# Optimization experiments

Hardware: AMD Instinct MI355X
Metric: run time of the kernel (lower is better)

Reference implementation:

```python
import jax, jax.numpy as jnp
import numpy as np
from jax import lax

DN = ('NCHW', 'OIHW', 'NCHW')


def conv2d(x, w, b, stride, pad):
    y = lax.conv_general_dilated(x, w, (stride, stride), [(pad, pad), (pad, pad)],
                                 dimension_numbers=DN)
    return y + b[None, :, None, None]


def conv2d_transpose(x, w, b):
    # k=4, s=2, p=1 transposed conv: lhs_dilation=2, padding k-1-p=2.
    # w is stored directly as OIHW for this dilated conv (reference params).
    y = lax.conv_general_dilated(x, w, (1, 1), [(2, 2), (2, 2)],
                                 lhs_dilation=(2, 2), dimension_numbers=DN)
    return y + b[None, :, None, None]


def setup_inputs() -> dict:
    key = jax.random.key(0)
    ks = jax.random.split(key, 16)
    D, K = 64, 512  # embedding_dim, num_embeddings
    C1, C2 = 128, 256

    def w(k, shape, fan_in):
        return (jax.random.normal(k, shape, jnp.float32) / np.sqrt(fan_in)).astype(jnp.float32)

    inp = {
        'x':   jax.random.normal(ks[0], (8, 3, 256, 256), jnp.float32),
        # encoder: two stride-2 conv stages (k=4,s=2,p=1) + ReLU
        'ew1': w(ks[1], (C1, 3, 4, 4), 3 * 16),   'eb1': jnp.zeros((C1,), jnp.float32),
        'ew2': w(ks[2], (C2, C1, 4, 4), C1 * 16), 'eb2': jnp.zeros((C2,), jnp.float32),
        # pre_vq 1x1 conv: C2 -> D
        'pvw': w(ks[3], (D, C2, 1, 1), C2),       'pvb': jnp.zeros((D,), jnp.float32),
        # codebook, uniform(-1/K, 1/K) as in the torch init
        'emb': jax.random.uniform(ks[4], (K, D), jnp.float32, -1.0 / K, 1.0 / K),
        # post_vq 3x3 conv: D -> C2
        'qvw': w(ks[5], (C2, D, 3, 3), D * 9),    'qvb': jnp.zeros((C2,), jnp.float32),
        # decoder: two stride-2 transposed conv stages
        'dw1': w(ks[6], (C1, C2, 4, 4), C2 * 16), 'db1': jnp.zeros((C1,), jnp.float32),
        'dw2': w(ks[7], (3, C1, 4, 4), C1 * 16),  'db2': jnp.zeros((3,), jnp.float32),
    }
    return inp


def vector_quantize(z_e, emb, commitment_cost):
    # z_e: [B, D, H, W] -> [B, H, W, D]
    inputs = jnp.transpose(z_e, (0, 2, 3, 1))
    B, H, W, D = inputs.shape
    K = emb.shape[0]
    flat = inputs.reshape(-1, D)                                   # [N, D]
    dist = (jnp.sum(flat * flat, axis=1, keepdims=True)
            + jnp.sum(emb * emb, axis=1)
            - 2.0 * jnp.matmul(flat, emb.T))                        # [N, K]
    idx = jnp.argmin(dist, axis=1)                                  # [N]
    encodings = jax.nn.one_hot(idx, K, dtype=flat.dtype)            # [N, K]
    quantized = emb[idx].reshape(B, H, W, D)                        # gather == encodings @ emb

    e_latent_loss = jnp.mean((lax.stop_gradient(quantized) - inputs) ** 2)
    q_latent_loss = jnp.mean((quantized - lax.stop_gradient(inputs)) ** 2)
    loss = q_latent_loss + commitment_cost * e_latent_loss

    quantized_st = inputs + lax.stop_gradient(quantized - inputs)   # straight-through
    avg_probs = jnp.mean(encodings, axis=0)
    perplexity = jnp.exp(-jnp.sum(avg_probs * jnp.log(avg_probs + 1e-10)))
    return loss, jnp.transpose(quantized_st, (0, 3, 1, 2)), perplexity, encodings


def reference(x, ew1, eb1, ew2, eb2, pvw, pvb, emb, qvw, qvb, dw1, db1, dw2, db2):
    commitment_cost = 0.25
    # encode
    h = jax.nn.relu(conv2d(x, ew1, eb1, 2, 1))    # [8,128,128,128]
    h = jax.nn.relu(conv2d(h, ew2, eb2, 2, 1))    # [8,256,64,64]
    z_e = conv2d(h, pvw, pvb, 1, 0)               # [8,64,64,64]
    # vector quantize
    loss, quantized, perplexity, _ = vector_quantize(z_e, emb, commitment_cost)
    # decode
    g = conv2d(quantized, qvw, qvb, 1, 1)         # [8,256,64,64]
    g = jax.nn.relu(conv2d_transpose(g, dw1, db1))  # [8,128,128,128]
    x_recon = conv2d_transpose(g, dw2, db2)       # [8,3,256,256]
    return (loss, x_recon, perplexity)
```

## Files before the change

kernel.cpp:

```cpp
#include <hip/hip_runtime.h>
#include <math.h>

typedef unsigned short u16;
typedef unsigned int uint;
typedef __attribute__((ext_vector_type(8))) short bh8;
typedef __attribute__((ext_vector_type(4))) float f32x4;

#define DEV __device__ __forceinline__

DEV u16 f2bf(float x) {
  uint u = __builtin_bit_cast(uint, x);
  return (u16)((u + 0x7FFFu + ((u >> 16) & 1u)) >> 16);
}
DEV float bf2f(u16 h) { return __builtin_bit_cast(float, (uint)h << 16); }

DEV int xcd_swz(int bid, int nb) {
  int c = nb >> 3;
  return (bid & 7) * c + (bid >> 3);
}

__global__ __launch_bounds__(256, 2) void conv1_mfma3(const float* __restrict__ src,
                                                      const u16* __restrict__ B1h,
                                                      const u16* __restrict__ B1l,
                                                      const float* __restrict__ bias,
                                                      uint* __restrict__ outu) {
  __shared__ __align__(16) u16 Ah[128*72 + 32];
  __shared__ __align__(16) u16 Al[128*72 + 32];
  __shared__ __align__(16) u16 Bh[128*72 + 32];
  __shared__ __align__(16) u16 Bl[128*72 + 32];

  const int t = threadIdx.x;
  const int mt = xcd_swz((int)blockIdx.x, (int)gridDim.x);
  const int pl = t & 127, kb = t >> 7;
  const int p = mt*128 + pl;
  const int n = p >> 14, h = (p >> 7) & 127, w = p & 127;
  const int lane = t & 63, wv = t >> 6;
  const int lr = lane & 15, lg = lane >> 4;
  const int wm = wv & 1, wn = wv >> 1;

  uint hi16[16], lo16[16];
  #pragma unroll
  for (int q = 0; q < 16; ++q) {
    uint hh = 0, ll = 0;
    #pragma unroll
    for (int e = 0; e < 2; ++e) {
      const int k = kb*32 + q*2 + e;
      float val = 0.f;
      if (k < 48) {
        const int ic = k >> 4, r = k & 15;
        const int ih = 2*h - 1 + (r >> 2), iw = 2*w - 1 + (r & 3);
        if ((unsigned)ih < 256u && (unsigned)iw < 256u)
          val = src[((n*3 + ic) << 16) + (ih << 8) + iw];
      }
      u16 hi = f2bf(val);
      u16 lo = f2bf(val - bf2f(hi));
      hh |= (uint)hi << (16*e);
      ll |= (uint)lo << (16*e);
    }
    hi16[q] = hh; lo16[q] = ll;
  }
  const int aw = pl*72 + kb*32;
  #pragma unroll
  for (int i = 0; i < 4; ++i) {
    *(uint4*)&Ah[aw + i*8] = *(uint4*)&hi16[4*i];
    *(uint4*)&Al[aw + i*8] = *(uint4*)&lo16[4*i];
  }
  #pragma unroll
  for (int i = 0; i < 4; ++i) {
    int id = i*256 + t, oc = id >> 3, ch = id & 7;
    *(uint4*)&Bh[oc*72 + ch*8] = *(const uint4*)(B1h + (size_t)oc*64 + ch*8);
    *(uint4*)&Bl[oc*72 + ch*8] = *(const uint4*)(B1l + (size_t)oc*64 + ch*8);
  }
  __syncthreads();

  f32x4 acc[4][4];
  #pragma unroll
  for (int fm = 0; fm < 4; ++fm)
    #pragma unroll
    for (int fn = 0; fn < 4; ++fn)
      #pragma unroll
      for (int q = 0; q < 4; ++q) acc[fm][fn][q] = 0.f;

  #pragma unroll
  for (int ks = 0; ks < 2; ++ks) {
    bh8 afh[4], afl[4];
    #pragma unroll
    for (int fm = 0; fm < 4; ++fm) {
      const int r = (wm*64 + fm*16 + lr)*72 + ks*32 + lg*8;
      afh[fm] = *(const bh8*)&Ah[r];
      afl[fm] = *(const bh8*)&Al[r];
    }
    #pragma unroll
    for (int fn = 0; fn < 4; ++fn) {
      const int r = (wn*64 + fn*16 + lr)*72 + ks*32 + lg*8;
      bh8 bfh = *(const bh8*)&Bh[r];
      bh8 bfl = *(const bh8*)&Bl[r];
      #pragma unroll
      for (int fm = 0; fm < 4; ++fm) {
        acc[fm][fn] = __builtin_amdgcn_mfma_f32_16x16x32_bf16(afh[fm], bfh, acc[fm][fn], 0,0,0);
        acc[fm][fn] = __builtin_amdgcn_mfma_f32_16x16x32_bf16(afl[fm], bfh, acc[fm][fn], 0,0,0);
        acc[fm][fn] = __builtin_amdgcn_mfma_f32_16x16x32_bf16(afh[fm], bfl, acc[fm][fn], 0,0,0);
      }
    }
  }

  #pragma unroll
  for (int fm = 0; fm < 4; ++fm) {
    const int pq = mt*128 + wm*64 + fm*16 + lg*4;
    const int nn = pq >> 14, hh2 = (pq >> 7) & 127, ww = pq & 127;
    const int wh = ww >> 1;
    #pragma unroll
    for (int fn = 0; fn < 4; ++fn) {
      const int oc = wn*64 + fn*16 + lr;
      const float bv = bias[oc];
      uint pk[4];
      #pragma unroll
      for (int q = 0; q < 4; ++q) {
        float v = fmaxf(acc[fm][fn][q] + bv, 0.f);
        u16 hi = f2bf(v);
        u16 lo = f2bf(v - bf2f(hi));
        pk[q] = (uint)hi | ((uint)lo << 16);
      }
      uint* bp = outu + (size_t)(nn*128 + oc)*16384 + hh2*128;
      *(uint2*)(bp + wh)      = make_uint2(pk[0], pk[2]);
      *(uint2*)(bp + 64 + wh) = make_uint2(pk[1], pk[3]);
    }
  }
}

__global__ __launch_bounds__(256, 2) void conv2_mfma3(const uint* __restrict__ h1u,
                                                      const u16* __restrict__ Bh,
                                                      const u16* __restrict__ Bl,
                                                      const float* __restrict__ bias,
                                                      float* __restrict__ out) {
  __shared__ __align__(16) u16 Ah[128*72 + 32];
  __shared__ __align__(16) u16 Al[128*72 + 32];
  __shared__ __align__(16) u16 Bhs[128*72 + 32];
  __shared__ __align__(16) u16 Bls[128*72 + 32];

  const int t = threadIdx.x;
  const int bid = xcd_swz((int)blockIdx.x, (int)gridDim.x);
  const int nt = bid & 1, mt = bid >> 1;
  const int pl = t & 127, kb = t >> 7;
  const int p = mt*128 + pl;
  const int n = p >> 12, h = (p >> 6) & 63, w = p & 63;
  const int lane = t & 63, wv = t >> 6;
  const int lr = lane & 15, lg = lane >> 4;
  const int wm = wv & 1, wn = wv >> 1;

  int off[4]; uint mskd[4];
  off[0] = 64 + w - 1; mskd[0] = (w >= 1)  ? ~0u : 0u;
  off[1] = w;          mskd[1] = ~0u;
  off[2] = 64 + w;     mskd[2] = ~0u;
  off[3] = w + 1;      mskd[3] = (w <= 62) ? ~0u : 0u;

  f32x4 acc[4][4];
  #pragma unroll
  for (int fm = 0; fm < 4; ++fm)
    #pragma unroll
    for (int fn = 0; fn < 4; ++fn)
      #pragma unroll
      for (int q = 0; q < 4; ++q) acc[fm][fn][q] = 0.f;

  const int aw = pl*72 + kb*32;

  for (int k0 = 0; k0 < 2048; k0 += 64) {
    const int dy = k0 >> 9, icb = (k0 >> 2) & 127;
    const int ih = 2*h - 1 + dy;
    const uint mih = ((unsigned)ih < 128u) ? ~0u : 0u;
    const uint* pb = h1u + (size_t)(n*128 + icb + kb*8)*16384
                        + (((unsigned)ih < 128u) ? ih : 0)*128;
    uint m2[4];
    #pragma unroll
    for (int dx = 0; dx < 4; ++dx) m2[dx] = mskd[dx] & mih;

    uint raw[32];
    #pragma unroll
    for (int c = 0; c < 8; ++c)
      #pragma unroll
      for (int dx = 0; dx < 4; ++dx)
        raw[c*4 + dx] = pb[c*16384 + off[dx]] & m2[dx];

    uint hi16[16], lo16[16];
    #pragma unroll
    for (int q = 0; q < 16; ++q) {
      uint a = raw[2*q], b = raw[2*q+1];
      hi16[q] = (a & 0xffffu) | (b << 16);
      lo16[q] = (a >> 16) | (b & 0xffff0000u);
    }
    __syncthreads();
    #pragma unroll
    for (int i = 0; i < 4; ++i) {
      *(uint4*)&Ah[aw + i*8] = *(uint4*)&hi16[4*i];
      *(uint4*)&Al[aw + i*8] = *(uint4*)&lo16[4*i];
    }
    #pragma unroll
    for (int i = 0; i < 4; ++i) {
      int id = i*256 + t, oc = id >> 3, ch = id & 7;
      size_t bo = (size_t)(nt*128 + oc)*2048 + k0 + ch*8;
      *(uint4*)&Bhs[oc*72 + ch*8] = *(const uint4*)(Bh + bo);
      *(uint4*)&Bls[oc*72 + ch*8] = *(const uint4*)(Bl + bo);
    }
    __syncthreads();

    #pragma unroll
    for (int ks = 0; ks < 2; ++ks) {
      bh8 afh[4], afl[4];
      #pragma unroll
      for (int fm = 0; fm < 4; ++fm) {
        const int r = (wm*64 + fm*16 + lr)*72 + ks*32 + lg*8;
        afh[fm] = *(const bh8*)&Ah[r];
        afl[fm] = *(const bh8*)&Al[r];
      }
      #pragma unroll
      for (int fn = 0; fn < 4; ++fn) {
        const int r = (wn*64 + fn*16 + lr)*72 + ks*32 + lg*8;
        bh8 bfh = *(const bh8*)&Bhs[r];
        bh8 bfl = *(const bh8*)&Bls[r];
        #pragma unroll
        for (int fm = 0; fm < 4; ++fm) {
          acc[fm][fn] = __builtin_amdgcn_mfma_f32_16x16x32_bf16(afh[fm], bfh, acc[fm][fn], 0,0,0);
          acc[fm][fn] = __builtin_amdgcn_mfma_f32_16x16x32_bf16(afl[fm], bfh, acc[fm][fn], 0,0,0);
          acc[fm][fn] = __builtin_amdgcn_mfma_f32_16x16x32_bf16(afh[fm], bfl, acc[fm][fn], 0,0,0);
        }
      }
    }
  }

  #pragma unroll
  for (int fm = 0; fm < 4; ++fm) {
    const int pq = mt*128 + wm*64 + fm*16 + lg*4;
    const int nn = pq >> 12, hwq = pq & 4095;
    #pragma unroll
    for (int fn = 0; fn < 4; ++fn) {
      const int oc = nt*128 + wn*64 + fn*16 + lr;
      const float bv = bias[oc];
      float v0 = fmaxf(acc[fm][fn][0] + bv, 0.f);
      float v1 = fmaxf(acc[fm][fn][1] + bv, 0.f);
      float v2 = fmaxf(acc[fm][fn][2] + bv, 0.f);
      float v3 = fmaxf(acc[fm][fn][3] + bv, 0.f);
      *(float4*)(out + (((size_t)(nn*256 + oc)) << 12) + hwq) = make_float4(v0,v1,v2,v3);
    }
  }
}

__global__ __launch_bounds__(256, 2) void prevq_vq(const float* __restrict__ h2,
                                                   const float* __restrict__ btp,
                                                   const float* __restrict__ pvb,
                                                   const float* __restrict__ emb,
                                                   const u16* __restrict__ Ebh,
                                                   const u16* __restrict__ Ebl,
                                                   const float* __restrict__ enrm,
                                                   uint* __restrict__ qz32,
                                                   int* __restrict__ hist,
                                                   float* __restrict__ loss_sum) {
  __shared__ __align__(16) char SMEM[75776];
  float* Zs    = (float*)SMEM;
  u16*   Zh    = (u16*)(SMEM + 17408);
  u16*   Zl    = (u16*)(SMEM + 26624);
  u16*   Eh    = (u16*)(SMEM + 35840);
  u16*   El    = (u16*)(SMEM + 54272);
  float* nrmS  = (float*)(SMEM + 72704);
  float* wredv = (float*)(SMEM + 73216);
  int*   wredi = (int*)(SMEM + 74240);
  int*   sIdx  = (int*)(SMEM + 75264);
  float* As    = (float*)(SMEM + 35840);
  float* Bs    = (float*)(SMEM + 35840 + 4096);

  const int t = threadIdx.x;
  const int base = (int)blockIdx.x * 64;
  const int n = base >> 12, hwb = base & 4095;
  const int ti = t & 15, tj = t >> 4;

  {
    const int pl = t & 63, kb = t >> 6;
    const int hw = hwb + pl;
    float acc[4][4];
    #pragma unroll
    for (int i = 0; i < 4; ++i)
      #pragma unroll
      for (int j = 0; j < 4; ++j) acc[i][j] = 0.f;

    for (int k0 = 0; k0 < 256; k0 += 16) {
      #pragma unroll
      for (int jj = 0; jj < 4; ++jj) {
        int kr = jj*4 + kb;
        As[kr*64 + pl] = h2[((size_t)(n*256 + k0 + kr) << 12) + hw];
      }
      {
        int kr = t >> 4, c4 = t & 15;
        ((float4*)Bs)[kr*16 + c4] = *((const float4*)(btp + (size_t)(k0 + kr)*64) + c4);
      }
      __syncthreads();
      #pragma unroll
      for (int kk = 0; kk < 16; ++kk) {
        float a[4], b[4];
        *(float4*)&a[0] = *(const float4*)&As[kk*64 + ti*4];
        *(float4*)&b[0] = *(const float4*)&Bs[kk*64 + tj*4];
        #pragma unroll
        for (int i = 0; i < 4; ++i)
          #pragma unroll
          for (int j = 0; j < 4; ++j)
            acc[i][j] += a[i]*b[j];
      }
      __syncthreads();
    }
    #pragma unroll
    for (int j = 0; j < 4; ++j) {
      const int d = tj*4 + j;
      const float bvv = pvb[d];
      #pragma unroll
      for (int i = 0; i < 4; ++i) {
        const int px = ti*4 + i;
        float z = acc[i][j] + bvv;
        Zs[d*68 + px] = z;
        u16 h = f2bf(z);
        Zh[px*72 + d] = h;
        Zl[px*72 + d] = f2bf(z - bf2f(h));
      }
    }
  }

  const int lane = t & 63, wv = t >> 6;
  const int lr = lane & 15, lg = lane >> 4;

  float bv2[4][4]; int bi2[4][4];
  #pragma unroll
  for (int fm = 0; fm < 4; ++fm)
    #pragma unroll
    for (int q = 0; q < 4; ++q) { bv2[fm][q] = 3.402823466e38f; bi2[fm][q] = 0; }

  for (int c = 0; c < 4; ++c) {
    __syncthreads();
    #pragma unroll
    for (int i = 0; i < 4; ++i) {
      int id = i*256 + t, row = id >> 3, ch = id & 7;
      *(uint4*)&Eh[row*72 + ch*8] = *(const uint4*)(Ebh + (size_t)(c*128 + row)*64 + ch*8);
      *(uint4*)&El[row*72 + ch*8] = *(const uint4*)(Ebl + (size_t)(c*128 + row)*64 + ch*8);
    }
    if (t < 128) nrmS[t] = enrm[c*128 + t];
    __syncthreads();

    f32x4 acc2[4][2];
    #pragma unroll
    for (int fm = 0; fm < 4; ++fm)
      #pragma unroll
      for (int fn = 0; fn < 2; ++fn)
        #pragma unroll
        for (int q = 0; q < 4; ++q) acc2[fm][fn][q] = 0.f;

    #pragma unroll
    for (int ks = 0; ks < 2; ++ks) {
      bh8 ah[4], al[4];
      #pragma unroll
      for (int fm = 0; fm < 4; ++fm) {
        const int r = (fm*16 + lr)*72 + ks*32 + lg*8;
        ah[fm] = *(const bh8*)&Zh[r];
        al[fm] = *(const bh8*)&Zl[r];
      }
      #pragma unroll
      for (int fn = 0; fn < 2; ++fn) {
        const int r = (wv*32 + fn*16 + lr)*72 + ks*32 + lg*8;
        bh8 bh_ = *(const bh8*)&Eh[r];
        bh8 bl_ = *(const bh8*)&El[r];
        #pragma unroll
        for (int fm = 0; fm < 4; ++fm) {
          acc2[fm][fn] = __builtin_amdgcn_mfma_f32_16x16x32_bf16(ah[fm], bh_, acc2[fm][fn], 0,0,0);
          acc2[fm][fn] = __builtin_amdgcn_mfma_f32_16x16x32_bf16(al[fm], bh_, acc2[fm][fn], 0,0,0);
          acc2[fm][fn] = __builtin_amdgcn_mfma_f32_16x16x32_bf16(ah[fm], bl_, acc2[fm][fn], 0,0,0);
        }
      }
    }
    #pragma unroll
    for (int fn = 0; fn < 2; ++fn) {
      const int code = c*128 + wv*32 + fn*16 + lr;
      const float nv = nrmS[wv*32 + fn*16 + lr];
      #pragma unroll
      for (int fm = 0; fm < 4; ++fm)
        #pragma unroll
        for (int q = 0; q < 4; ++q) {
          float d = nv - 2.f*acc2[fm][fn][q];
          if (d < bv2[fm][q]) { bv2[fm][q] = d; bi2[fm][q] = code; }
        }
    }
  }

  #pragma unroll
  for (int fm = 0; fm < 4; ++fm)
    #pragma unroll
    for (int q = 0; q < 4; ++q) {
      float v = bv2[fm][q]; int ix = bi2[fm][q];
      #pragma unroll
      for (int m = 1; m < 16; m <<= 1) {
        float ov = __shfl_xor(v, m, 64);
        int   oi = __shfl_xor(ix, m, 64);
        if (ov < v || (ov == v && oi < ix)) { v = ov; ix = oi; }
      }
      if (lr == 0) {
        const int px = fm*16 + lg*4 + q;
        wredv[wv*64 + px] = v;
        wredi[wv*64 + px] = ix;
      }
    }
  __syncthreads();
  if (t < 64) {
    float best = 3.402823466e38f; int bid = 0x7fffffff;
    #pragma unroll
    for (int w2 = 0; w2 < 4; ++w2) {
      float v = wredv[w2*64 + t]; int ix = wredi[w2*64 + t];
      if (v < best || (v == best && ix < bid)) { best = v; bid = ix; }
    }
    sIdx[t] = bid;
  }
  __syncthreads();

  const int px = t & 63, grp = t >> 6;
  const int ix = sIdx[px];
  const float* er = emb + (size_t)ix * 64 + grp*16;
  uint* qb = qz32 + ((size_t)(n*32 + grp*8))*4096 + hwb + px;
  float ls = 0.f;
  #pragma unroll
  for (int dp = 0; dp < 8; ++dp) {
    float e0 = er[2*dp], e1 = er[2*dp + 1];
    float z0 = Zs[(grp*16 + 2*dp)*68 + px];
    float z1 = Zs[(grp*16 + 2*dp + 1)*68 + px];
    float d0 = e0 - z0, d1 = e1 - z1;
    ls += d0*d0 + d1*d1;
    qb[(size_t)dp * 4096] = (uint)f2bf(e0) | ((uint)f2bf(e1) << 16);
  }
  if (t < 64) atomicAdd(&hist[ix], 1);
  #pragma unroll
  for (int o = 32; o; o >>= 1) ls += __shfl_down(ls, o, 64);
  if ((t & 63) == 0) atomicAdd(loss_sum, ls);
}

__global__ void finalize_kernel(const int* __restrict__ hist,
                                const float* __restrict__ loss_sum,
                                float* __restrict__ out_loss,
                                float* __restrict__ out_perp) {
  __shared__ float red[512];
  int t = threadIdx.x;
  float pr = (float)hist[t] * (1.f/32768.f);
  red[t] = pr * logf(pr + 1e-10f);
  __syncthreads();
  for (int s = 256; s; s >>= 1) {
    if (t < s) red[t] += red[t + s];
    __syncthreads();
  }
  if (t == 0) {
    out_loss[0] = 1.25f * loss_sum[0] * (1.f/2097152.f);
    out_perp[0] = expf(-red[0]);
  }
}

enum { M_POSTVQ, M_DECONV1, M_DECONV2 };

template<int MODE>
__global__ __launch_bounds__(256, 4) void dec_mfma128(const uint* __restrict__ srcu,
                                                      const u16* __restrict__ Bt,
                                                      const float* __restrict__ bias,
                                                      uint* __restrict__ out32) {
  constexpr int K = (MODE == M_POSTVQ) ? 576 : 1024;
  __shared__ __align__(16) u16 As[128*72 + 32];
  __shared__ __align__(16) u16 Bs[128*72 + 32];

  const int t = threadIdx.x;
  int bid = xcd_swz((int)blockIdx.x, (int)gridDim.x);
  int par = 0, nt = 0, mt;
  if constexpr (MODE == M_DECONV1) { par = bid & 3; mt = bid >> 2; }
  else                             { nt = bid & 1;  mt = bid >> 1; }
  const u16* Brow = Bt + (size_t)((MODE == M_DECONV1) ? par*128 : nt*128) * K;

  const int pl = t & 127, kb = t >> 7;
  const int p = mt*128 + pl;
  const int n = p >> 12, h = (p >> 6) & 63, w = p & 63;
  const int lane = t & 63, wv = t >> 6;
  const int lr = lane & 15, lg = lane >> 4;
  const int wm = wv & 1, wn = wv >> 1;

  f32x4 acc[4][4];
  #pragma unroll
  for (int fm = 0; fm < 4; ++fm)
    #pragma unroll
    for (int fn = 0; fn < 4; ++fn)
      #pragma unroll
      for (int q = 0; q < 4; ++q) acc[fm][fn][q] = 0.f;

  const int aw = pl*72 + kb*32;

  for (int k0 = 0; k0 < K; k0 += 64) {
    const uint* up; bool ok;
    if constexpr (MODE == M_POSTVQ) {
      int r = k0 >> 6, kh = r / 3, kw = r - 3*kh;
      int ih = h - 1 + kh, iw = w - 1 + kw;
      ok = ((unsigned)ih < 64u) && ((unsigned)iw < 64u);
      up = srcu + ((size_t)(n*32 + kb*16)) * 4096
                + (ok ? ((ih << 6) + iw) : 0);
    } else {
      int j = k0 >> 8, icb = k0 & 255;
      int j1 = j >> 1, j0 = j & 1;
      int py = par >> 1, px = par & 1;
      int ih = h + py - 1 + j1, iw = w + px - 1 + j0;
      ok = ((unsigned)ih < 64u) && ((unsigned)iw < 64u);
      up = srcu + ((size_t)(n*128 + (icb >> 1) + kb*16)) * 4096
                + (ok ? ((ih << 6) + iw) : 0);
    }
    uint raw[16];
    #pragma unroll
    for (int i = 0; i < 16; ++i)
      raw[i] = ok ? up[(size_t)i * 4096] : 0u;

    __syncthreads();
    #pragma unroll
    for (int i = 0; i < 4; ++i)
      *(uint4*)&As[aw + i*8] =
          make_uint4(raw[4*i], raw[4*i+1], raw[4*i+2], raw[4*i+3]);

    #pragma unroll
    for (int i = 0; i < 4; ++i) {
      int id = i*256 + t, oc = id >> 3, ch = id & 7;
      *(uint4*)&Bs[oc*72 + ch*8] = *(const uint4*)(Brow + (size_t)oc*K + k0 + ch*8);
    }
    __syncthreads();

    #pragma unroll
    for (int ks = 0; ks < 2; ++ks) {
      bh8 af[4];
      #pragma unroll
      for (int fm = 0; fm < 4; ++fm)
        af[fm] = *(const bh8*)&As[(wm*64 + fm*16 + lr)*72 + ks*32 + lg*8];
      #pragma unroll
      for (int fn = 0; fn < 4; ++fn) {
        bh8 bf = *(const bh8*)&Bs[(wn*64 + fn*16 + lr)*72 + ks*32 + lg*8];
        #pragma unroll
        for (int fm = 0; fm < 4; ++fm)
          acc[fm][fn] = __builtin_amdgcn_mfma_f32_16x16x32_bf16(af[fm], bf, acc[fm][fn], 0, 0, 0);
      }
    }
  }

  const bool evn = !(lr & 1);
  #pragma unroll
  for (int fm = 0; fm < 4; ++fm) {
    const int pq = mt*128 + wm*64 + fm*16 + lg*4;
    const int nn = pq >> 12, hwq = pq & 4095;
    #pragma unroll
    for (int fn = 0; fn < 4; ++fn) {
      const int oc = nt*128 + wn*64 + fn*16 + lr;
      const float bvv = bias[oc];
      float v[4];
      #pragma unroll
      for (int q = 0; q < 4; ++q) {
        v[q] = acc[fm][fn][q] + bvv;
        if constexpr (MODE == M_DECONV1) v[q] = fmaxf(v[q], 0.f);
      }
      float pv[4];
      #pragma unroll
      for (int q = 0; q < 4; ++q) pv[q] = __shfl_xor(v[q], 1, 64);
      uint pk[4];
      #pragma unroll
      for (int q = 0; q < 4; ++q) {
        u16 a = f2bf(evn ? v[q] : pv[q]);
        u16 b = f2bf(evn ? pv[q] : v[q]);
        pk[q] = (uint)a | ((uint)b << 16);
      }
      size_t pbase;
      if constexpr (MODE == M_POSTVQ)
        pbase = ((size_t)(nn*128 + (oc >> 1))) * 4096 + hwq;
      else
        pbase = ((size_t)((nn*4 + par)*64 + (oc >> 1))) * 4096 + hwq;
      if (evn) *(uint2*)(out32 + pbase)     = make_uint2(pk[0], pk[1]);
      else     *(uint2*)(out32 + pbase + 2) = make_uint2(pk[2], pk[3]);
    }
  }
}

__global__ __launch_bounds__(256, 4) void deconv2_mfma(const uint* __restrict__ srcu,
                                                       const u16* __restrict__ Bt,
                                                       const float* __restrict__ bias,
                                                       float* __restrict__ outf) {
  constexpr int K = 512, BN = 16;
  __shared__ __align__(16) u16 As[128 * 72];
  __shared__ __align__(16) u16 Bs[BN * 72];

  const int t = threadIdx.x;
  int bid = xcd_swz((int)blockIdx.x, (int)gridDim.x);
  int par = bid & 3; bid >>= 2;
  const int mt = bid;
  const u16* Brow = Bt + (size_t)par * BN * K;

  const int pl = t & 127, kb = t >> 7;
  const int p = mt * 128 + pl;
  const int n = p >> 14, h = (p >> 7) & 127, w = p & 127;

  const int lane = t & 63, wv = t >> 6;
  const int lr = lane & 15, lg = lane >> 4;

  f32x4 acc[2];
  #pragma unroll
  for (int fm = 0; fm < 2; ++fm)
    #pragma unroll
    for (int q = 0; q < 4; ++q) acc[fm][q] = 0.f;

  for (int k0 = 0; k0 < K; k0 += 64) {
    int tap = k0 >> 7, icb = k0 & 127;
    int j1 = tap >> 1, j0 = tap & 1;
    int qy = par >> 1, qx = par & 1;
    int ih = h - 1 + qy + j1, iw = w - 1 + qx + j0;
    bool ok = ((unsigned)ih < 128u) && ((unsigned)iw < 128u);
    int ipar = ((ih & 1) << 1) | (iw & 1);
    const uint* up = srcu + ((size_t)((n*4 + ipar)*64 + (icb >> 1) + kb*16)) * 4096
                          + (ok ? (((ih >> 1) << 6) + (iw >> 1)) : 0);
    uint raw[16];
    #pragma unroll
    for (int i = 0; i < 16; ++i)
      raw[i] = ok ? up[(size_t)i * 4096] : 0u;

    __syncthreads();
    #pragma unroll
    for (int i = 0; i < 4; ++i)
      *(uint4*)&As[pl*72 + kb*32 + i*8] =
          make_uint4(raw[4*i], raw[4*i+1], raw[4*i+2], raw[4*i+3]);
    {
      int id = t;
      if (id < BN*8) {
        int oc = id >> 3, ch = id & 7;
        *(uint4*)&Bs[oc*72 + ch*8] = *(const uint4*)(Brow + (size_t)oc*K + k0 + ch*8);
      }
    }
    __syncthreads();

    #pragma unroll
    for (int ks = 0; ks < 2; ++ks) {
      bh8 af[2];
      #pragma unroll
      for (int fm = 0; fm < 2; ++fm)
        af[fm] = *(const bh8*)&As[(wv*32 + fm*16 + lr)*72 + ks*32 + lg*8];
      bh8 bf = *(const bh8*)&Bs[lr*72 + ks*32 + lg*8];
      #pragma unroll
      for (int fm = 0; fm < 2; ++fm)
        acc[fm] = __builtin_amdgcn_mfma_f32_16x16x32_bf16(af[fm], bf, acc[fm], 0, 0, 0);
    }
  }

  #pragma unroll
  for (int fm = 0; fm < 2; ++fm) {
    const int pq = mt*128 + wv*32 + fm*16 + lg*4;
    const int oc = lr;
    if (oc < 3) {
      const float bvv = bias[oc];
      const int nn = pq >> 14;
      const int hq = (pq >> 7) & 127, wq = pq & 127;
      const int qy = par >> 1, qx = par & 1;
      const int oh = 2*hq + qy;
      float* ob = outf + (((size_t)(nn*3 + oc)) << 16) + (oh << 8) + qx;
      ob[2*wq]     = acc[fm][0] + bvv;
      ob[2*wq + 2] = acc[fm][1] + bvv;
      ob[2*wq + 4] = acc[fm][2] + bvv;
      ob[2*wq + 6] = acc[fm][3] + bvv;
    }
  }
}

__global__ void prep_all(const float* __restrict__ ew1, const float* __restrict__ ew2,
                         const float* __restrict__ pvw, const float* __restrict__ emb,
                         const float* __restrict__ qvw, const float* __restrict__ dw1,
                         const float* __restrict__ dw2,
                         u16* bt1h, u16* bt1l, u16* bt2h, u16* bt2l, float* btp,
                         u16* Ebh, u16* Ebl, float* enrm,
                         u16* btq, u16* btd, u16* btd2,
                         int* hist, float* lsum) {
  int i = blockIdx.x * 256 + threadIdx.x;
  if (i < 8192) {
    int oc = i >> 6, k = i & 63;
    float v = (k < 48) ? ew1[oc*48 + k] : 0.f;
    u16 hi = f2bf(v);
    bt1h[i] = hi;
    bt1l[i] = f2bf(v - bf2f(hi));
  } else if ((i -= 8192) < 524288) {
    int oc = i >> 11, k = i & 2047;
    int dy = k >> 9, ic = (k >> 2) & 127, dx = k & 3;
    float v = ew2[oc*2048 + ic*16 + dy*4 + dx];
    u16 hi = f2bf(v);
    bt2h[i] = hi;
    bt2l[i] = f2bf(v - bf2f(hi));
  } else if ((i -= 524288) < 16384) {
    int k = i >> 6, oc = i & 63;
    btp[i] = pvw[oc*256 + k];
  } else if ((i -= 16384) < 32768) {
    float v = emb[i];
    u16 hi = f2bf(v);
    Ebh[i] = hi;
    Ebl[i] = f2bf(v - bf2f(hi));
  } else if ((i -= 32768) < 512) {
    float s = 0.f;
    const float* er = emb + (size_t)i * 64;
    #pragma unroll
    for (int d = 0; d < 64; ++d) s += er[d]*er[d];
    enrm[i] = s;
  } else if ((i -= 512) < 147456) {
    int oc = i / 576, rem = i - oc*576, r = rem >> 6, ic = rem & 63;
    btq[i] = f2bf(qvw[oc*576 + ic*9 + r]);
  } else if ((i -= 147456) < 524288) {
    int pr = i >> 17, oc = (i >> 10) & 127, j = (i >> 8) & 3, ic = i & 255;
    int py = pr >> 1, px = pr & 1, j1 = j >> 1, j0 = j & 1;
    btd[i] = f2bf(dw1[oc*4096 + ic*16 + (py + 2*j1)*4 + (px + 2*j0)]);
  } else if ((i -= 524288) < 32768) {
    int q = i >> 13, oc = (i >> 9) & 15, tap = (i >> 7) & 3, ic = i & 127;
    int qy = q >> 1, qx = q & 1, j1 = tap >> 1, j0 = tap & 1;
    btd2[i] = (oc < 3) ? f2bf(dw2[oc*2048 + ic*16 + (qy + 2*j1)*4 + (qx + 2*j0)]) : (u16)0;
  } else if ((i -= 32768) < 528) {
    if (i < 512) hist[i] = 0;
    else         lsum[i - 512] = 0.f;
  }
}

extern "C" void kernel_launch(void* const* d_in, const int* in_sizes, int n_in,
                              void* d_out, int out_size, void* d_ws, size_t ws_size,
                              hipStream_t stream) {
  (void)in_sizes; (void)n_in; (void)ws_size;
  const float* x   = (const float*)d_in[0];
  const float* ew1 = (const float*)d_in[1];
  const float* eb1 = (const float*)d_in[2];
  const float* ew2 = (const float*)d_in[3];
  const float* eb2 = (const float*)d_in[4];
  const float* pvw = (const float*)d_in[5];
  const float* pvb = (const float*)d_in[6];
  const float* emb = (const float*)d_in[7];
  const float* qvw = (const float*)d_in[8];
  const float* qvb = (const float*)d_in[9];
  const float* dw1 = (const float*)d_in[10];
  const float* db1 = (const float*)d_in[11];
  const float* dw2 = (const float*)d_in[12];
  const float* db2 = (const float*)d_in[13];
  float* out = (float*)d_out;

  char* ws = (char*)d_ws;
  uint*  h1u  = (uint*) (ws);
  float* h2   = (float*)(ws + 67108864);
  uint*  qz32 = (uint*) (ws + 109051904);
  int*   hist = (int*)  (ws + 113246208);
  float* lsum = (float*)(ws + 113248256);
  u16*   bt1h = (u16*)  (ws + 113248320);
  u16*   bt1l = (u16*)  (ws + 113264704);
  float* btp  = (float*)(ws + 113281088);
  u16*   bt2h = (u16*)  (ws + 113346624);
  u16*   bt2l = (u16*)  (ws + 114395200);
  u16*   btq  = (u16*)  (ws + 115443776);
  u16*   btd  = (u16*)  (ws + 115738688);
  u16*   btd2 = (u16*)  (ws + 116787264);
  u16*   Ebh  = (u16*)  (ws + 116852800);
  u16*   Ebl  = (u16*)  (ws + 116918336);
  float* enrm = (float*)(ws + 116983872);
  uint* g32  = (uint*)(ws + 67108864);
  uint* g232 = (uint*)ws;

  prep_all<<<5029, 256, 0, stream>>>(ew1, ew2, pvw, emb, qvw, dw1, dw2,
                                     bt1h, bt1l, bt2h, bt2l, btp,
                                     Ebh, Ebl, enrm, btq, btd, btd2, hist, lsum);

  conv1_mfma3<<<1024, 256, 0, stream>>>(x, bt1h, bt1l, eb1, h1u);
  conv2_mfma3<<<512, 256, 0, stream>>>(h1u, bt2h, bt2l, eb2, h2);

  prevq_vq<<<512, 256, 0, stream>>>(h2, btp, pvb, emb, Ebh, Ebl, enrm, qz32, hist, lsum);
  finalize_kernel<<<1, 512, 0, stream>>>(hist, lsum, out, out + (out_size - 1));

  dec_mfma128<M_POSTVQ> <<<512,  256, 0, stream>>>(qz32, btq, qvb, g32);
  dec_mfma128<M_DECONV1><<<1024, 256, 0, stream>>>(g32, btd, db1, g232);
  deconv2_mfma<<<4096, 256, 0, stream>>>(g232, btd2, db2, out + 1);
}
```

Measured before the change: 378.1 us.

## Run pre-VQ 1x1 conv on split-bf16 MFMA with packed hi/lo conv2 output

```diff
diff --git a/kernel.cpp b/kernel.cpp
--- a/kernel.cpp
+++ b/kernel.cpp
@@ -132,7 +132,7 @@
                                                       const u16* __restrict__ Bh,
                                                       const u16* __restrict__ Bl,
                                                       const float* __restrict__ bias,
-                                                      float* __restrict__ out) {
+                                                      uint* __restrict__ outh2) {
   __shared__ __align__(16) u16 Ah[128*72 + 32];
   __shared__ __align__(16) u16 Al[128*72 + 32];
   __shared__ __align__(16) u16 Bhs[128*72 + 32];
@@ -235,17 +235,23 @@
     for (int fn = 0; fn < 4; ++fn) {
       const int oc = nt*128 + wn*64 + fn*16 + lr;
       const float bv = bias[oc];
-      float v0 = fmaxf(acc[fm][fn][0] + bv, 0.f);
-      float v1 = fmaxf(acc[fm][fn][1] + bv, 0.f);
-      float v2 = fmaxf(acc[fm][fn][2] + bv, 0.f);
-      float v3 = fmaxf(acc[fm][fn][3] + bv, 0.f);
-      *(float4*)(out + (((size_t)(nn*256 + oc)) << 12) + hwq) = make_float4(v0,v1,v2,v3);
-    }
-  }
-}
-
-__global__ __launch_bounds__(256, 2) void prevq_vq(const float* __restrict__ h2,
-                                                   const float* __restrict__ btp,
+      uint pk[4];
+      #pragma unroll
+      for (int q = 0; q < 4; ++q) {
+        float v = fmaxf(acc[fm][fn][q] + bv, 0.f);
+        u16 hi = f2bf(v);
+        u16 lo = f2bf(v - bf2f(hi));
+        pk[q] = (uint)hi | ((uint)lo << 16);
+      }
+      *(uint4*)(outh2 + (((size_t)(nn*256 + oc)) << 12) + hwq) =
+          make_uint4(pk[0], pk[1], pk[2], pk[3]);
+    }
+  }
+}
+
+__global__ __launch_bounds__(256, 2) void prevq_vq(const uint* __restrict__ h2u,
+                                                   const u16* __restrict__ btph,
+                                                   const u16* __restrict__ btpl,
                                                    const float* __restrict__ pvb,
                                                    const float* __restrict__ emb,
                                                    const u16* __restrict__ Ebh,
@@ -258,71 +264,85 @@
   float* Zs    = (float*)SMEM;
   u16*   Zh    = (u16*)(SMEM + 17408);
   u16*   Zl    = (u16*)(SMEM + 26624);
+  u16*   A1h   = (u16*)(SMEM + 35840);
+  u16*   A1l   = (u16*)(SMEM + 45056);
+  u16*   B1h   = (u16*)(SMEM + 54272);
+  u16*   B1l   = (u16*)(SMEM + 63488);
   u16*   Eh    = (u16*)(SMEM + 35840);
   u16*   El    = (u16*)(SMEM + 54272);
   float* nrmS  = (float*)(SMEM + 72704);
   float* wredv = (float*)(SMEM + 73216);
   int*   wredi = (int*)(SMEM + 74240);
   int*   sIdx  = (int*)(SMEM + 75264);
-  float* As    = (float*)(SMEM + 35840);
-  float* Bs    = (float*)(SMEM + 35840 + 4096);
 
   const int t = threadIdx.x;
   const int base = (int)blockIdx.x * 64;
   const int n = base >> 12, hwb = base & 4095;
-  const int ti = t & 15, tj = t >> 4;
-
-  {
-    const int pl = t & 63, kb = t >> 6;
-    const int hw = hwb + pl;
-    float acc[4][4];
-    #pragma unroll
-    for (int i = 0; i < 4; ++i)
-      #pragma unroll
-      for (int j = 0; j < 4; ++j) acc[i][j] = 0.f;
-
-    for (int k0 = 0; k0 < 256; k0 += 16) {
-      #pragma unroll
-      for (int jj = 0; jj < 4; ++jj) {
-        int kr = jj*4 + kb;
-        As[kr*64 + pl] = h2[((size_t)(n*256 + k0 + kr) << 12) + hw];
-      }
-      {
-        int kr = t >> 4, c4 = t & 15;
-        ((float4*)Bs)[kr*16 + c4] = *((const float4*)(btp + (size_t)(k0 + kr)*64) + c4);
-      }
-      __syncthreads();
-      #pragma unroll
-      for (int kk = 0; kk < 16; ++kk) {
-        float a[4], b[4];
-        *(float4*)&a[0] = *(const float4*)&As[kk*64 + ti*4];
-        *(float4*)&b[0] = *(const float4*)&Bs[kk*64 + tj*4];
-        #pragma unroll
-        for (int i = 0; i < 4; ++i)
-          #pragma unroll
-          for (int j = 0; j < 4; ++j)
-            acc[i][j] += a[i]*b[j];
-      }
-      __syncthreads();
-    }
-    #pragma unroll
-    for (int j = 0; j < 4; ++j) {
-      const int d = tj*4 + j;
-      const float bvv = pvb[d];
-      #pragma unroll
-      for (int i = 0; i < 4; ++i) {
-        const int px = ti*4 + i;
-        float z = acc[i][j] + bvv;
-        Zs[d*68 + px] = z;
-        u16 h = f2bf(z);
-        Zh[px*72 + d] = h;
-        Zl[px*72 + d] = f2bf(z - bf2f(h));
-      }
-    }
-  }
-
   const int lane = t & 63, wv = t >> 6;
   const int lr = lane & 15, lg = lane >> 4;
+
+  {
+    const int px = t & 63, kb = t >> 6;
+    f32x4 acc1[4];
+    #pragma unroll
+    for (int fm = 0; fm < 4; ++fm)
+      #pragma unroll
+      for (int q = 0; q < 4; ++q) acc1[fm][q] = 0.f;
+
+    for (int k0 = 0; k0 < 256; k0 += 64) {
+      const uint* pb = h2u + ((size_t)(n*256 + k0 + kb*16)) * 4096 + hwb + px;
+      uint raw[16];
+      #pragma unroll
+      for (int c = 0; c < 16; ++c) raw[c] = pb[(size_t)c * 4096];
+      uint hi8[8], lo8[8];
+      #pragma unroll
+      for (int q = 0; q < 8; ++q) {
+        uint a = raw[2*q], b = raw[2*q+1];
+        hi8[q] = (a & 0xffffu) | (b << 16);
+        lo8[q] = (a >> 16) | (b & 0xffff0000u);
+      }
+      __syncthreads();
+      const int aw = px*72 + kb*16;
+      *(uint4*)&A1h[aw]     = *(uint4*)&hi8[0];
+      *(uint4*)&A1h[aw + 8] = *(uint4*)&hi8[4];
+      *(uint4*)&A1l[aw]     = *(uint4*)&lo8[0];
+      *(uint4*)&A1l[aw + 8] = *(uint4*)&lo8[4];
+      #pragma unroll
+      for (int i = 0; i < 2; ++i) {
+        int id = i*256 + t, d = id >> 3, ch = id & 7;
+        *(uint4*)&B1h[d*72 + ch*8] = *(const uint4*)(btph + (size_t)d*256 + k0 + ch*8);
+        *(uint4*)&B1l[d*72 + ch*8] = *(const uint4*)(btpl + (size_t)d*256 + k0 + ch*8);
+      }
+      __syncthreads();
+
+      #pragma unroll
+      for (int ks = 0; ks < 2; ++ks) {
+        bh8 bh_ = *(const bh8*)&B1h[(wv*16 + lr)*72 + ks*32 + lg*8];
+        bh8 bl_ = *(const bh8*)&B1l[(wv*16 + lr)*72 + ks*32 + lg*8];
+        #pragma unroll
+        for (int fm = 0; fm < 4; ++fm) {
+          bh8 ah = *(const bh8*)&A1h[(fm*16 + lr)*72 + ks*32 + lg*8];
+          bh8 al = *(const bh8*)&A1l[(fm*16 + lr)*72 + ks*32 + lg*8];
+          acc1[fm] = __builtin_amdgcn_mfma_f32_16x16x32_bf16(ah, bh_, acc1[fm], 0,0,0);
+          acc1[fm] = __builtin_amdgcn_mfma_f32_16x16x32_bf16(al, bh_, acc1[fm], 0,0,0);
+          acc1[fm] = __builtin_amdgcn_mfma_f32_16x16x32_bf16(ah, bl_, acc1[fm], 0,0,0);
+        }
+      }
+    }
+    const int d = wv*16 + lr;
+    const float bvv = pvb[d];
+    #pragma unroll
+    for (int fm = 0; fm < 4; ++fm)
+      #pragma unroll
+      for (int q = 0; q < 4; ++q) {
+        const int pxo = fm*16 + lg*4 + q;
+        float z = acc1[fm][q] + bvv;
+        Zs[d*68 + pxo] = z;
+        u16 hh = f2bf(z);
+        Zh[pxo*72 + d] = hh;
+        Zl[pxo*72 + d] = f2bf(z - bf2f(hh));
+      }
+  }
 
   float bv2[4][4]; int bi2[4][4];
   #pragma unroll
@@ -666,7 +686,8 @@
                          const float* __restrict__ pvw, const float* __restrict__ emb,
                          const float* __restrict__ qvw, const float* __restrict__ dw1,
                          const float* __restrict__ dw2,
-                         u16* bt1h, u16* bt1l, u16* bt2h, u16* bt2l, float* btp,
+                         u16* bt1h, u16* bt1l, u16* bt2h, u16* bt2l,
+                         u16* btph, u16* btpl,
                          u16* Ebh, u16* Ebl, float* enrm,
                          u16* btq, u16* btd, u16* btd2,
                          int* hist, float* lsum) {
@@ -685,8 +706,10 @@
     bt2h[i] = hi;
     bt2l[i] = f2bf(v - bf2f(hi));
   } else if ((i -= 524288) < 16384) {
-    int k = i >> 6, oc = i & 63;
-    btp[i] = pvw[oc*256 + k];
+    float v = pvw[i];
+    u16 hi = f2bf(v);
+    btph[i] = hi;
+    btpl[i] = f2bf(v - bf2f(hi));
   } else if ((i -= 16384) < 32768) {
     float v = emb[i];
     u16 hi = f2bf(v);
@@ -737,13 +760,14 @@
 
   char* ws = (char*)d_ws;
   uint*  h1u  = (uint*) (ws);
-  float* h2   = (float*)(ws + 67108864);
+  uint*  h2u  = (uint*) (ws + 67108864);
   uint*  qz32 = (uint*) (ws + 109051904);
   int*   hist = (int*)  (ws + 113246208);
   float* lsum = (float*)(ws + 113248256);
   u16*   bt1h = (u16*)  (ws + 113248320);
   u16*   bt1l = (u16*)  (ws + 113264704);
-  float* btp  = (float*)(ws + 113281088);
+  u16*   btph = (u16*)  (ws + 113281088);
+  u16*   btpl = (u16*)  (ws + 113313856);
   u16*   bt2h = (u16*)  (ws + 113346624);
   u16*   bt2l = (u16*)  (ws + 114395200);
   u16*   btq  = (u16*)  (ws + 115443776);
@@ -756,13 +780,14 @@
   uint* g232 = (uint*)ws;
 
   prep_all<<<5029, 256, 0, stream>>>(ew1, ew2, pvw, emb, qvw, dw1, dw2,
-                                     bt1h, bt1l, bt2h, bt2l, btp,
+                                     bt1h, bt1l, bt2h, bt2l, btph, btpl,
                                      Ebh, Ebl, enrm, btq, btd, btd2, hist, lsum);
 
   conv1_mfma3<<<1024, 256, 0, stream>>>(x, bt1h, bt1l, eb1, h1u);
-  conv2_mfma3<<<512, 256, 0, stream>>>(h1u, bt2h, bt2l, eb2, h2);
-
-  prevq_vq<<<512, 256, 0, stream>>>(h2, btp, pvb, emb, Ebh, Ebl, enrm, qz32, hist, lsum);
+  conv2_mfma3<<<512, 256, 0, stream>>>(h1u, bt2h, bt2l, eb2, h2u);
+
+  prevq_vq<<<512, 256, 0, stream>>>(h2u, btph, btpl, pvb, emb, Ebh, Ebl, enrm,
+                                    qz32, hist, lsum);
   finalize_kernel<<<1, 512, 0, stream>>>(hist, lsum, out, out + (out_size - 1));
 
   dec_mfma128<M_POSTVQ> <<<512,  256, 0, stream>>>(qz32, btq, qvb, g32);
```

Measured after the change: 368.7 us. 1.03x faster.
